# Kernel optimization log

Hardware: AMD Instinct MI355X
Metric: run time of the kernel (lower is better)

## Reference

```python
import jax, jax.numpy as jnp
import numpy as np

NUM_EXPERTS = 8
HIDDEN = 1024
INTER = 2048
TOKENS = 4096
INIT_STD = 0.02


def setup_inputs() -> dict:
    key = jax.random.key(0)
    k1, k2, k3, k4 = jax.random.split(key, 4)
    return {
        "hidden_states": jax.random.normal(k1, (TOKENS, HIDDEN), jnp.float32),
        "gate_kernel": jax.random.normal(k2, (NUM_EXPERTS, HIDDEN, INTER), jnp.float32) * INIT_STD,
        "up_kernel": jax.random.normal(k3, (NUM_EXPERTS, HIDDEN, INTER), jnp.float32) * INIT_STD,
        "down_kernel": jax.random.normal(k4, (NUM_EXPERTS, INTER, HIDDEN), jnp.float32) * INIT_STD,
        # tokens are pre-sorted by expert; equal-sized groups summing to TOKENS
        "group_sizes": jnp.full((NUM_EXPERTS,), TOKENS // NUM_EXPERTS, dtype=jnp.int32),
    }


def reference(hidden_states, gate_kernel, up_kernel, down_kernel, group_sizes):
    # Grouped (ragged) GEMM expert FFN with SwiGLU:
    #   y = ragged_dot(silu(x @ Wg[e]) * (x @ Wu[e]), Wd[e])
    # hidden_states: [T, H] sorted by expert, group_sizes: [E]
    gate = jax.lax.ragged_dot(hidden_states, gate_kernel, group_sizes)  # [T, I]
    up = jax.lax.ragged_dot(hidden_states, up_kernel, group_sizes)      # [T, I]
    return jax.lax.ragged_dot(jax.nn.silu(gate) * up, down_kernel, group_sizes)  # [T, H]
```

## Files before the change

### kernel.cpp

```cpp
#include <hip/hip_runtime.h>
#include <hip/hip_bf16.h>

#define DEVI static __device__ __forceinline__

typedef __attribute__((ext_vector_type(8))) short bf16x8;
typedef __attribute__((ext_vector_type(4))) float f32x4;
typedef __attribute__((ext_vector_type(4))) int i32x4;
typedef __attribute__((ext_vector_type(2))) unsigned u32x2;

constexpr int NE = 8;
constexpr int HID = 1024;
constexpr int INTER = 2048;
constexpr int BM = 64, BN = 64, BK = 64;

DEVI int swz(int r, int c) { return (r * BK + c) ^ ((r & 7) << 3); }

DEVI short f2bf(float f) {
  union { float f; unsigned u; } v;
  v.f = f;
  unsigned r = v.u + 0x7FFFu + ((v.u >> 16) & 1u);
  return (short)(r >> 16);
}

DEVI u32x2 pack4(float a, float b, float c, float d) {
  u32x2 o;
  o[0] = (unsigned)(unsigned short)f2bf(a) | ((unsigned)(unsigned short)f2bf(b) << 16);
  o[1] = (unsigned)(unsigned short)f2bf(c) | ((unsigned)(unsigned short)f2bf(d) << 16);
  return o;
}

__global__ __launch_bounds__(256, 2) void gate_up_kernel(
    const float* __restrict__ x, const float* __restrict__ wg,
    const float* __restrict__ wu, const int* __restrict__ gsz,
    short* __restrict__ act) {
  const int e = blockIdx.z;
  int row_start = 0;
  for (int i = 0; i < e; ++i) row_start += gsz[i];
  const int rows = gsz[e];
  const int m0 = blockIdx.y * BM;
  if (m0 >= rows) return;
  const int n0 = blockIdx.x * BN;
  const int row_lim = rows - m0;

  __shared__ __align__(16) short As[2][BM * BK];
  __shared__ __align__(16) short Bgs[2][BN * BK];
  __shared__ __align__(16) short Bus[2][BN * BK];

  const int tid = threadIdx.x;
  const int l = tid & 63;
  const int wid = tid >> 6;
  const int wr = (wid >> 1) * 32;
  const int wc = (wid & 1) * 32;
  const int lr = l & 15;
  const int kb = (l >> 4) * 8;

  const float* xa = x + (size_t)(row_start + m0) * HID;
  const float* wga = wg + (size_t)e * HID * INTER + n0;
  const float* wua = wu + (size_t)e * HID * INTER + n0;

  const int ar = tid >> 4;
  const int ac = (tid & 15) * 4;
  const int bn4 = tid & 15;
  const int bkq = tid >> 4;
  const int lrot = tid & 3;

  f32x4 ra[4], rbg[4], rbu[4];

  auto load_tile = [&](int k0) {
#pragma unroll
    for (int it = 0; it < 4; ++it) {
      int r = ar + it * 16;
      int rr = r < row_lim ? r : row_lim - 1;
      ra[it] = *reinterpret_cast<const f32x4*>(xa + (size_t)rr * HID + k0 + ac);
    }
    const float* pg = wga + (size_t)(k0 + bkq * 4) * INTER + bn4 * 4;
    const float* pu = wua + (size_t)(k0 + bkq * 4) * INTER + bn4 * 4;
#pragma unroll
    for (int j = 0; j < 4; ++j) rbg[j] = *reinterpret_cast<const f32x4*>(pg + (size_t)j * INTER);
#pragma unroll
    for (int j = 0; j < 4; ++j) rbu[j] = *reinterpret_cast<const f32x4*>(pu + (size_t)j * INTER);
  };

  auto write_tile = [&](int buf) {
    short* As_ = As[buf];
    short* Bg_ = Bgs[buf];
    short* Bu_ = Bus[buf];
#pragma unroll
    for (int it = 0; it < 4; ++it) {
      int r = ar + it * 16;
      *reinterpret_cast<u32x2*>(&As_[swz(r, ac)]) =
          pack4(ra[it][0], ra[it][1], ra[it][2], ra[it][3]);
    }
#pragma unroll
    for (int ii = 0; ii < 4; ++ii) {
      int i = (ii + lrot) & 3;
      *reinterpret_cast<u32x2*>(&Bg_[swz(bn4 * 4 + i, bkq * 4)]) =
          pack4(rbg[0][i], rbg[1][i], rbg[2][i], rbg[3][i]);
    }
#pragma unroll
    for (int ii = 0; ii < 4; ++ii) {
      int i = (ii + lrot) & 3;
      *reinterpret_cast<u32x2*>(&Bu_[swz(bn4 * 4 + i, bkq * 4)]) =
          pack4(rbu[0][i], rbu[1][i], rbu[2][i], rbu[3][i]);
    }
  };

  f32x4 accg[2][2] = {};
  f32x4 accu[2][2] = {};

  constexpr int NT = HID / BK;
  load_tile(0);
  write_tile(0);
  __syncthreads();

  for (int kt = 0; kt < NT; ++kt) {
    if (kt + 1 < NT) load_tile((kt + 1) * BK);
    const short* As_ = As[kt & 1];
    const short* Bg_ = Bgs[kt & 1];
    const short* Bu_ = Bus[kt & 1];
#pragma unroll
    for (int kk = 0; kk < BK; kk += 32) {
      bf16x8 a[2], bg[2], bu[2];
#pragma unroll
      for (int mi = 0; mi < 2; ++mi)
        a[mi] = *reinterpret_cast<const bf16x8*>(&As_[swz(wr + mi * 16 + lr, kk + kb)]);
#pragma unroll
      for (int ni = 0; ni < 2; ++ni) {
        bg[ni] = *reinterpret_cast<const bf16x8*>(&Bg_[swz(wc + ni * 16 + lr, kk + kb)]);
        bu[ni] = *reinterpret_cast<const bf16x8*>(&Bu_[swz(wc + ni * 16 + lr, kk + kb)]);
      }
#pragma unroll
      for (int mi = 0; mi < 2; ++mi)
#pragma unroll
        for (int ni = 0; ni < 2; ++ni) {
          accg[mi][ni] = __builtin_amdgcn_mfma_f32_16x16x32_bf16(a[mi], bg[ni], accg[mi][ni], 0, 0, 0);
          accu[mi][ni] = __builtin_amdgcn_mfma_f32_16x16x32_bf16(a[mi], bu[ni], accu[mi][ni], 0, 0, 0);
        }
    }
    if (kt + 1 < NT) write_tile((kt + 1) & 1);
    __syncthreads();
  }

  short* actp = act + (size_t)(row_start + m0) * INTER + n0;
#pragma unroll
  for (int mi = 0; mi < 2; ++mi) {
#pragma unroll
    for (int r = 0; r < 4; ++r) {
      int rloc = wr + mi * 16 + (l >> 4) * 4 + r;
      if (rloc < row_lim) {
#pragma unroll
        for (int ni = 0; ni < 2; ++ni) {
          float g = accg[mi][ni][r];
          float u = accu[mi][ni][r];
          float s = g / (1.0f + __expf(-g));
          actp[(size_t)rloc * INTER + wc + ni * 16 + lr] = f2bf(s * u);
        }
      }
    }
  }
}

__global__ __launch_bounds__(256, 2) void down_kernel(
    const short* __restrict__ act, const float* __restrict__ wd,
    const int* __restrict__ gsz, float* __restrict__ out) {
  const int e = blockIdx.z;
  int row_start = 0;
  for (int i = 0; i < e; ++i) row_start += gsz[i];
  const int rows = gsz[e];
  const int m0 = blockIdx.y * BM;
  if (m0 >= rows) return;
  const int n0 = blockIdx.x * BN;
  const int row_lim = rows - m0;

  __shared__ __align__(16) short As[2][BM * BK];
  __shared__ __align__(16) short Bs[2][BN * BK];

  const int tid = threadIdx.x;
  const int l = tid & 63;
  const int wid = tid >> 6;
  const int wr = (wid >> 1) * 32;
  const int wc = (wid & 1) * 32;
  const int lr = l & 15;
  const int kb = (l >> 4) * 8;

  const short* aa = act + (size_t)(row_start + m0) * INTER;
  const float* wda = wd + (size_t)e * INTER * HID + n0;

  const int ar = (tid >> 3);
  const int ac = (tid & 7) * 8;
  const int bn4 = tid & 15;
  const int bkq = tid >> 4;
  const int lrot = tid & 3;

  i32x4 raa[2];
  f32x4 rb[4];

  auto load_tile = [&](int k0) {
#pragma unroll
    for (int it = 0; it < 2; ++it) {
      int r = ar + it * 32;
      int rr = r < row_lim ? r : row_lim - 1;
      raa[it] = *reinterpret_cast<const i32x4*>(aa + (size_t)rr * INTER + k0 + ac);
    }
    const float* pb = wda + (size_t)(k0 + bkq * 4) * HID + bn4 * 4;
#pragma unroll
    for (int j = 0; j < 4; ++j) rb[j] = *reinterpret_cast<const f32x4*>(pb + (size_t)j * HID);
  };

  auto write_tile = [&](int buf) {
    short* As_ = As[buf];
    short* Bs_ = Bs[buf];
#pragma unroll
    for (int it = 0; it < 2; ++it) {
      int r = ar + it * 32;
      *reinterpret_cast<i32x4*>(&As_[swz(r, ac)]) = raa[it];
    }
#pragma unroll
    for (int ii = 0; ii < 4; ++ii) {
      int i = (ii + lrot) & 3;
      *reinterpret_cast<u32x2*>(&Bs_[swz(bn4 * 4 + i, bkq * 4)]) =
          pack4(rb[0][i], rb[1][i], rb[2][i], rb[3][i]);
    }
  };

  f32x4 acc[2][2] = {};

  constexpr int NT = INTER / BK;
  load_tile(0);
  write_tile(0);
  __syncthreads();

  for (int kt = 0; kt < NT; ++kt) {
    if (kt + 1 < NT) load_tile((kt + 1) * BK);
    const short* As_ = As[kt & 1];
    const short* Bs_ = Bs[kt & 1];
#pragma unroll
    for (int kk = 0; kk < BK; kk += 32) {
      bf16x8 a[2], b[2];
#pragma unroll
      for (int mi = 0; mi < 2; ++mi)
        a[mi] = *reinterpret_cast<const bf16x8*>(&As_[swz(wr + mi * 16 + lr, kk + kb)]);
#pragma unroll
      for (int ni = 0; ni < 2; ++ni)
        b[ni] = *reinterpret_cast<const bf16x8*>(&Bs_[swz(wc + ni * 16 + lr, kk + kb)]);
#pragma unroll
      for (int mi = 0; mi < 2; ++mi)
#pragma unroll
        for (int ni = 0; ni < 2; ++ni)
          acc[mi][ni] = __builtin_amdgcn_mfma_f32_16x16x32_bf16(a[mi], b[ni], acc[mi][ni], 0, 0, 0);
    }
    if (kt + 1 < NT) write_tile((kt + 1) & 1);
    __syncthreads();
  }

  float* outp = out + (size_t)(row_start + m0) * HID + n0;
#pragma unroll
  for (int mi = 0; mi < 2; ++mi) {
#pragma unroll
    for (int r = 0; r < 4; ++r) {
      int rloc = wr + mi * 16 + (l >> 4) * 4 + r;
      if (rloc < row_lim) {
#pragma unroll
        for (int ni = 0; ni < 2; ++ni)
          outp[(size_t)rloc * HID + wc + ni * 16 + lr] = acc[mi][ni][r];
      }
    }
  }
}

extern "C" void kernel_launch(void* const* d_in, const int* in_sizes, int n_in,
                              void* d_out, int out_size, void* d_ws, size_t ws_size,
                              hipStream_t stream) {
  const float* x = (const float*)d_in[0];
  const float* wg = (const float*)d_in[1];
  const float* wu = (const float*)d_in[2];
  const float* wd = (const float*)d_in[3];
  const int* gsz = (const int*)d_in[4];
  float* out = (float*)d_out;
  short* act = (short*)d_ws;

  const int T = in_sizes[0] / HID;
  const int mtiles = (T + BM - 1) / BM;

  dim3 blk(256, 1, 1);
  gate_up_kernel<<<dim3(INTER / BN, mtiles, NE), blk, 0, stream>>>(x, wg, wu, gsz, act);
  down_kernel<<<dim3(HID / BN, mtiles, NE), blk, 0, stream>>>(act, wd, gsz, out);
}
```

Measured before the change: 336.7 us.

## Pre-convert weights and activations to bf16 and stream them via global_load_lds

Adds preprocessing kernels that convert x to bf16 and transpose-convert the three weight tensors to bf16 in workspace, K-major. New GEMM kernels then load tiles straight into LDS with global_load_lds, with no per-tile fp32-to-bf16 conversion in registers. The conversion passes read all fp32 weights once every call and write bf16 copies, which adds traffic and kernel launches. The old path is kept as a fallback when the workspace is too small.

```diff
diff --git a/kernel.cpp b/kernel.cpp
--- a/kernel.cpp
+++ b/kernel.cpp
@@ -27,6 +27,242 @@
   o[0] = (unsigned)(unsigned short)f2bf(a) | ((unsigned)(unsigned short)f2bf(b) << 16);
   o[1] = (unsigned)(unsigned short)f2bf(c) | ((unsigned)(unsigned short)f2bf(d) << 16);
   return o;
+}
+
+DEVI void gload16(const void* g, void* l) {
+  __builtin_amdgcn_global_load_lds((const __attribute__((address_space(1))) void*)g,
+                                   (__attribute__((address_space(3))) void*)l, 16, 0, 0);
+}
+
+
+__global__ __launch_bounds__(256) void convert_x_kernel(const float* __restrict__ in,
+                                                        short* __restrict__ out, int n) {
+  int idx = (blockIdx.x * 256 + threadIdx.x) * 8;
+  if (idx >= n) return;
+  f32x4 a = *reinterpret_cast<const f32x4*>(in + idx);
+  f32x4 b = *reinterpret_cast<const f32x4*>(in + idx + 4);
+  i32x4 o;
+  u32x2 p0 = pack4(a[0], a[1], a[2], a[3]);
+  u32x2 p1 = pack4(b[0], b[1], b[2], b[3]);
+  o[0] = p0[0]; o[1] = p0[1]; o[2] = p1[0]; o[3] = p1[1];
+  *reinterpret_cast<i32x4*>(out + idx) = o;
+}
+
+__global__ __launch_bounds__(256) void transpose_convert_kernel(
+    const float* __restrict__ src, short* __restrict__ dst, int K, int N) {
+  const int e = blockIdx.z;
+  const int N0 = blockIdx.x * 64;
+  const int K0 = blockIdx.y * 64;
+  __shared__ __align__(16) short L[64 * 72];
+
+  const int t = threadIdx.x;
+  const float* s = src + (size_t)e * K * N;
+  short* d = dst + (size_t)e * N * K;
+
+  {
+    int n4 = t & 15;
+    int kq = t >> 4;
+    const float* p = s + (size_t)(K0 + kq * 4) * N + N0 + n4 * 4;
+    f32x4 v[4];
+#pragma unroll
+    for (int j = 0; j < 4; ++j) v[j] = *reinterpret_cast<const f32x4*>(p + (size_t)j * N);
+    int lrot = t & 3;
+#pragma unroll
+    for (int ii = 0; ii < 4; ++ii) {
+      int i = (ii + lrot) & 3;
+      *reinterpret_cast<u32x2*>(&L[(n4 * 4 + i) * 72 + kq * 4]) =
+          pack4(v[0][i], v[1][i], v[2][i], v[3][i]);
+    }
+  }
+  __syncthreads();
+#pragma unroll
+  for (int it = 0; it < 2; ++it) {
+    int n = (t >> 3) + it * 32;
+    int kg = t & 7;
+    i32x4 v = *reinterpret_cast<const i32x4*>(&L[n * 72 + kg * 8]);
+    *reinterpret_cast<i32x4*>(d + (size_t)(N0 + n) * K + K0 + kg * 8) = v;
+  }
+}
+
+__global__ __launch_bounds__(256, 2) void gate_up_bf_kernel(
+    const short* __restrict__ x, const short* __restrict__ wgt,
+    const short* __restrict__ wut, const int* __restrict__ gsz,
+    short* __restrict__ act) {
+  const int e = blockIdx.z;
+  int row_start = 0;
+  for (int i = 0; i < e; ++i) row_start += gsz[i];
+  const int rows = gsz[e];
+  const int m0 = blockIdx.y * BM;
+  if (m0 >= rows) return;
+  const int n0 = blockIdx.x * BN;
+  const int row_lim = rows - m0;
+
+  __shared__ __align__(16) short As[2][BM * BK];
+  __shared__ __align__(16) short Bgs[2][BN * BK];
+  __shared__ __align__(16) short Bus[2][BN * BK];
+
+  const int tid = threadIdx.x;
+  const int l = tid & 63;
+  const int wid = tid >> 6;
+  const int wr = (wid >> 1) * 32;
+  const int wc = (wid & 1) * 32;
+  const int lr = l & 15;
+  const int kb = (l >> 4) * 8;
+
+  const short* xa = x + (size_t)(row_start + m0) * HID;
+  const short* wga = wgt + (size_t)e * INTER * HID + (size_t)n0 * HID;
+  const short* wua = wut + (size_t)e * INTER * HID + (size_t)n0 * HID;
+
+  auto stage = [&](int buf, int k0) {
+    short* As_ = As[buf];
+    short* Bg_ = Bgs[buf];
+    short* Bu_ = Bus[buf];
+#pragma unroll
+    for (int s = 0; s < 2; ++s) {
+      int r0 = wid * 16 + s * 8;
+      int r = r0 + (l >> 3);
+      int gg = (l & 7) ^ (r & 7);
+      int rr = r < row_lim ? r : row_lim - 1;
+      gload16(xa + (size_t)rr * HID + k0 + gg * 8, &As_[r0 * 64]);
+      gload16(wga + (size_t)r * HID + k0 + gg * 8, &Bg_[r0 * 64]);
+      gload16(wua + (size_t)r * HID + k0 + gg * 8, &Bu_[r0 * 64]);
+    }
+  };
+
+  f32x4 accg[2][2] = {};
+  f32x4 accu[2][2] = {};
+
+  constexpr int NT = HID / BK;
+  stage(0, 0);
+  __syncthreads();
+
+  for (int kt = 0; kt < NT; ++kt) {
+    if (kt + 1 < NT) stage((kt + 1) & 1, (kt + 1) * BK);
+    const short* As_ = As[kt & 1];
+    const short* Bg_ = Bgs[kt & 1];
+    const short* Bu_ = Bus[kt & 1];
+#pragma unroll
+    for (int kk = 0; kk < BK; kk += 32) {
+      bf16x8 a[2], bg[2], bu[2];
+#pragma unroll
+      for (int mi = 0; mi < 2; ++mi)
+        a[mi] = *reinterpret_cast<const bf16x8*>(&As_[swz(wr + mi * 16 + lr, kk + kb)]);
+#pragma unroll
+      for (int ni = 0; ni < 2; ++ni) {
+        bg[ni] = *reinterpret_cast<const bf16x8*>(&Bg_[swz(wc + ni * 16 + lr, kk + kb)]);
+        bu[ni] = *reinterpret_cast<const bf16x8*>(&Bu_[swz(wc + ni * 16 + lr, kk + kb)]);
+      }
+#pragma unroll
+      for (int mi = 0; mi < 2; ++mi)
+#pragma unroll
+        for (int ni = 0; ni < 2; ++ni) {
+          accg[mi][ni] = __builtin_amdgcn_mfma_f32_16x16x32_bf16(a[mi], bg[ni], accg[mi][ni], 0, 0, 0);
+          accu[mi][ni] = __builtin_amdgcn_mfma_f32_16x16x32_bf16(a[mi], bu[ni], accu[mi][ni], 0, 0, 0);
+        }
+    }
+    __syncthreads();
+  }
+
+  short* actp = act + (size_t)(row_start + m0) * INTER + n0;
+#pragma unroll
+  for (int mi = 0; mi < 2; ++mi) {
+#pragma unroll
+    for (int r = 0; r < 4; ++r) {
+      int rloc = wr + mi * 16 + (l >> 4) * 4 + r;
+      if (rloc < row_lim) {
+#pragma unroll
+        for (int ni = 0; ni < 2; ++ni) {
+          float g = accg[mi][ni][r];
+          float u = accu[mi][ni][r];
+          float s = g / (1.0f + __expf(-g));
+          actp[(size_t)rloc * INTER + wc + ni * 16 + lr] = f2bf(s * u);
+        }
+      }
+    }
+  }
+}
+
+__global__ __launch_bounds__(256, 2) void down_bf_kernel(
+    const short* __restrict__ act, const short* __restrict__ wdt,
+    const int* __restrict__ gsz, float* __restrict__ out) {
+  const int e = blockIdx.z;
+  int row_start = 0;
+  for (int i = 0; i < e; ++i) row_start += gsz[i];
+  const int rows = gsz[e];
+  const int m0 = blockIdx.y * BM;
+  if (m0 >= rows) return;
+  const int n0 = blockIdx.x * BN;
+  const int row_lim = rows - m0;
+
+  __shared__ __align__(16) short As[2][BM * BK];
+  __shared__ __align__(16) short Bs[2][BN * BK];
+
+  const int tid = threadIdx.x;
+  const int l = tid & 63;
+  const int wid = tid >> 6;
+  const int wr = (wid >> 1) * 32;
+  const int wc = (wid & 1) * 32;
+  const int lr = l & 15;
+  const int kb = (l >> 4) * 8;
+
+  const short* aa = act + (size_t)(row_start + m0) * INTER;
+  const short* wda = wdt + (size_t)e * HID * INTER + (size_t)n0 * INTER;
+
+  auto stage = [&](int buf, int k0) {
+    short* As_ = As[buf];
+    short* Bs_ = Bs[buf];
+#pragma unroll
+    for (int s = 0; s < 2; ++s) {
+      int r0 = wid * 16 + s * 8;
+      int r = r0 + (l >> 3);
+      int gg = (l & 7) ^ (r & 7);
+      int rr = r < row_lim ? r : row_lim - 1;
+      gload16(aa + (size_t)rr * INTER + k0 + gg * 8, &As_[r0 * 64]);
+      gload16(wda + (size_t)r * INTER + k0 + gg * 8, &Bs_[r0 * 64]);
+    }
+  };
+
+  f32x4 acc[2][2] = {};
+
+  constexpr int NT = INTER / BK;
+  stage(0, 0);
+  __syncthreads();
+
+  for (int kt = 0; kt < NT; ++kt) {
+    if (kt + 1 < NT) stage((kt + 1) & 1, (kt + 1) * BK);
+    const short* As_ = As[kt & 1];
+    const short* Bs_ = Bs[kt & 1];
+#pragma unroll
+    for (int kk = 0; kk < BK; kk += 32) {
+      bf16x8 a[2], b[2];
+#pragma unroll
+      for (int mi = 0; mi < 2; ++mi)
+        a[mi] = *reinterpret_cast<const bf16x8*>(&As_[swz(wr + mi * 16 + lr, kk + kb)]);
+#pragma unroll
+      for (int ni = 0; ni < 2; ++ni)
+        b[ni] = *reinterpret_cast<const bf16x8*>(&Bs_[swz(wc + ni * 16 + lr, kk + kb)]);
+#pragma unroll
+      for (int mi = 0; mi < 2; ++mi)
+#pragma unroll
+        for (int ni = 0; ni < 2; ++ni)
+          acc[mi][ni] = __builtin_amdgcn_mfma_f32_16x16x32_bf16(a[mi], b[ni], acc[mi][ni], 0, 0, 0);
+    }
+    __syncthreads();
+  }
+
+  float* outp = out + (size_t)(row_start + m0) * HID + n0;
+#pragma unroll
+  for (int mi = 0; mi < 2; ++mi) {
+#pragma unroll
+    for (int r = 0; r < 4; ++r) {
+      int rloc = wr + mi * 16 + (l >> 4) * 4 + r;
+      if (rloc < row_lim) {
+#pragma unroll
+        for (int ni = 0; ni < 2; ++ni)
+          outp[(size_t)rloc * HID + wc + ni * 16 + lr] = acc[mi][ni][r];
+      }
+    }
+  }
 }
 
 __global__ __launch_bounds__(256, 2) void gate_up_kernel(
@@ -277,12 +513,33 @@
   const float* wd = (const float*)d_in[3];
   const int* gsz = (const int*)d_in[4];
   float* out = (float*)d_out;
-  short* act = (short*)d_ws;
 
   const int T = in_sizes[0] / HID;
   const int mtiles = (T + BM - 1) / BM;
-
   dim3 blk(256, 1, 1);
-  gate_up_kernel<<<dim3(INTER / BN, mtiles, NE), blk, 0, stream>>>(x, wg, wu, gsz, act);
-  down_kernel<<<dim3(HID / BN, mtiles, NE), blk, 0, stream>>>(act, wd, gsz, out);
-}
+
+  const size_t XBF = (size_t)T * HID;
+  const size_t ACT = (size_t)T * INTER;
+  const size_t WT = (size_t)NE * HID * INTER;
+  const size_t NEED = (XBF + ACT + 3 * WT) * sizeof(short);
+
+  if (ws_size >= NEED) {
+    short* xbf = (short*)d_ws;
+    short* act = xbf + XBF;
+    short* wgt = act + ACT;
+    short* wut = wgt + WT;
+    short* wdt = wut + WT;
+
+    convert_x_kernel<<<(T * HID) / (256 * 8), blk, 0, stream>>>(x, xbf, T * HID);
+    transpose_convert_kernel<<<dim3(INTER / 64, HID / 64, NE), blk, 0, stream>>>(wg, wgt, HID, INTER);
+    transpose_convert_kernel<<<dim3(INTER / 64, HID / 64, NE), blk, 0, stream>>>(wu, wut, HID, INTER);
+    transpose_convert_kernel<<<dim3(HID / 64, INTER / 64, NE), blk, 0, stream>>>(wd, wdt, INTER, HID);
+
+    gate_up_bf_kernel<<<dim3(INTER / BN, mtiles, NE), blk, 0, stream>>>(xbf, wgt, wut, gsz, act);
+    down_bf_kernel<<<dim3(HID / BN, mtiles, NE), blk, 0, stream>>>(act, wdt, gsz, out);
+  } else {
+    short* act = (short*)d_ws;
+    gate_up_kernel<<<dim3(INTER / BN, mtiles, NE), blk, 0, stream>>>(x, wg, wu, gsz, act);
+    down_kernel<<<dim3(HID / BN, mtiles, NE), blk, 0, stream>>>(act, wd, gsz, out);
+  }
+}
```

Result: faster. 322.0 us (-4.4%).
